# Kernel tuning notes

Measured on AMD Instinct MI355X. Metric: run time of the kernel, lower is better.

The kernel has to match this reference:

```python
import jax, jax.numpy as jnp
import numpy as np

B, NQ, C = 4, 3136, 512
H_IMG, W_IMG = 56, 56
HEADS, D_MODEL, D_K, D_V = 8, 512, 512, 512
RATIO = 2
LN_EPS = 1e-3   # keras LayerNormalization default
BN_EPS = 1e-3   # keras BatchNormalization default


def setup_inputs() -> dict:
    key = jax.random.key(0)
    ks = jax.random.split(key, 16)
    s = 0.02
    inp = {
        'queries': jax.random.normal(ks[0], (B, NQ, C), jnp.float32),
        'keys': jax.random.normal(ks[1], (B, NQ, C), jnp.float32),
        'values': jax.random.normal(ks[2], (B, NQ, C), jnp.float32),
        'Wq': jax.random.normal(ks[3], (C, HEADS * D_K), jnp.float32) * s,
        'bq': jnp.zeros((HEADS * D_K,), jnp.float32),
        'Wk': jax.random.normal(ks[4], (C, HEADS * D_K), jnp.float32) * s,
        'bk': jnp.zeros((HEADS * D_K,), jnp.float32),
        'Wv': jax.random.normal(ks[5], (C, HEADS * D_V), jnp.float32) * s,
        'bv': jnp.zeros((HEADS * D_V,), jnp.float32),
        'Wo': jax.random.normal(ks[6], (HEADS * D_V, D_MODEL), jnp.float32) * s,
        'bo': jnp.zeros((D_MODEL,), jnp.float32),
        # depthwise conv: kernel (kh, kw, in_per_group=1, out=C)
        'sr_kernel': jax.random.normal(ks[7], (RATIO + 1, RATIO + 1, 1, C), jnp.float32) * s,
        'sr_bias': jnp.zeros((C,), jnp.float32),
        'ln_gamma': jnp.ones((C,), jnp.float32),
        'ln_beta': jnp.zeros((C,), jnp.float32),
        # 1x1 channels_first conv over the head axis of the score tensor
        'tw': jax.random.normal(ks[8], (HEADS, HEADS), jnp.float32) * s,
        'tb': jnp.zeros((HEADS,), jnp.float32),
        # BatchNormalization(axis=[0,1]) -> params per (batch, head)
        'bn_gamma': jnp.ones((B, HEADS), jnp.float32),
        'bn_beta': jnp.zeros((B, HEADS), jnp.float32),
    }
    return inp


def _forward(queries, keys, values, Wq, bq, Wk, bk, Wv, bv, Wo, bo,
             sr_kernel, sr_bias, ln_gamma, ln_beta, tw, tb, bn_gamma, bn_beta):
    b, nq, c = queries.shape
    # Q projection -> (b, h, nq, d_model)  (d_k == d_model)
    q = (queries @ Wq + bq).reshape(b, nq, HEADS, D_MODEL).transpose(0, 2, 1, 3)
    # spatial reduction of K/V source (ratio > 1 path; keys/values args unused)
    x = queries.reshape(b, H_IMG, W_IMG, c)
    x = jax.lax.conv_general_dilated(
        x, sr_kernel, window_strides=(RATIO, RATIO), padding='SAME',
        dimension_numbers=('NHWC', 'HWIO', 'NHWC'), feature_group_count=c) + sr_bias
    x = x.reshape(b, -1, c)  # (b, nk, c), nk = (H/ratio)*(W/ratio)
    mu = jnp.mean(x, axis=-1, keepdims=True)
    var = jnp.mean(jnp.square(x - mu), axis=-1, keepdims=True)
    x = (x - mu) * jax.lax.rsqrt(var + LN_EPS) * ln_gamma + ln_beta
    k = (x @ Wk + bk).reshape(b, -1, HEADS, D_MODEL).transpose(0, 2, 1, 3)
    v = (x @ Wv + bv).reshape(b, -1, HEADS, D_MODEL).transpose(0, 2, 1, 3)
    # scores (b, h, nq, nk)
    att = jnp.einsum('bhqd,bhkd->bhqk', q, k) / np.sqrt(D_K).astype(np.float32)
    # transform: 1x1 conv over head channel, softmax over k, BN over (q, k)
    att = jnp.einsum('bhqk,hg->bgqk', att, tw) + tb[:, None, None]
    att = jax.nn.softmax(att, axis=-1)
    m = jnp.mean(att, axis=(2, 3), keepdims=True)
    s2 = jnp.mean(jnp.square(att - m), axis=(2, 3), keepdims=True)
    att = bn_gamma[:, :, None, None] * (att - m) * jax.lax.rsqrt(s2 + BN_EPS) \
          + bn_beta[:, :, None, None]
    # attend and project out
    out = jnp.einsum('bhqk,bhkd->bhqd', att, v)
    out = out.transpose(0, 2, 1, 3).reshape(b, nq, HEADS * D_V)
    return out @ Wo + bo


def reference(queries, keys, values, Wq, bq, Wk, bk, Wv, bv, Wo, bo,
              sr_kernel, sr_bias, ln_gamma, ln_beta, tw, tb, bn_gamma, bn_beta):
    return _forward(queries, keys, values, Wq, bq, Wk, bk, Wv, bv, Wo, bo,
                    sr_kernel, sr_bias, ln_gamma, ln_beta, tw, tb, bn_gamma, bn_beta)
```

## Files before the change

### kernel.cpp

```cpp
#include <hip/hip_runtime.h>
#include <hip/hip_bf16.h>
#include <math.h>

typedef unsigned short u16;
typedef __attribute__((ext_vector_type(4))) float f32x4;
typedef __attribute__((ext_vector_type(8))) __bf16 bf16x8;

#define B_    4
#define NQ_   3136
#define C_    512
#define HIMG  56
#define WIMG  56
#define HD_   4096
#define NK_   784
#define NKP_  832

static __device__ __forceinline__ float b2f(u16 u){
  union { unsigned int i; float f; } v; v.i = ((unsigned int)u)<<16; return v.f;
}
static __device__ __forceinline__ u16 f2b(float f){
  union { float f; unsigned int i; } v; v.f = f;
  unsigned int r = v.i + 0x7fffu + ((v.i>>16)&1u);
  return (u16)(r>>16);
}

#define GLD16(gsrc, ldst) __builtin_amdgcn_global_load_lds( \
    (const __attribute__((address_space(1))) void*)(gsrc), \
    (__attribute__((address_space(3))) void*)(ldst), 16, 0, 0)

static __device__ __forceinline__ void xcd_swz(int &bx, int &by, int &bz){
  const long nx = gridDim.x, ny = gridDim.y, nz = gridDim.z;
  const long l = blockIdx.x + nx*(blockIdx.y + ny*(long)blockIdx.z);
  const long n = nx*ny*nz;
  const long q8 = n>>3, r8 = n&7;
  const long xcd = l&7, idx = l>>3;
  const long wg = (xcd<r8 ? xcd*(q8+1) : r8*(q8+1) + (xcd-r8)*q8) + idx;
  by = (int)(wg % ny);
  bx = (int)((wg/ny) % nx);
  bz = (int)(wg/(nx*ny));
}

template<int OUT_F32>
__global__ __launch_bounds__(256)
void gemm128(const u16* __restrict__ A, const u16* __restrict__ Bm, void* __restrict__ Cm,
             int M, int Ncols, int K, int sA, int sB, int sC, int zdiv,
             long long zA1, long long zA2, long long zB1, long long zB2,
             long long zC1, long long zC2,
             const float* __restrict__ bias1, float hscale,
             const float* __restrict__ scalePtr,
             const float* __restrict__ bias2, int rowsPerB, int b2s)
{
  __shared__ u16 lds[32768];
  int bx, by, z;
  xcd_swz(bx, by, z);
  const int zq = z / zdiv, zr = z % zdiv;
  const u16* Ab = A  + (long long)zq*zA1 + (long long)zr*zA2;
  const u16* Bb = Bm + (long long)zq*zB1 + (long long)zr*zB2;
  const int m0 = bx*128, n0 = by*128;
  const int t = threadIdx.x, w = t>>6, lane = t&63;
  const int wm = w>>1, wn = w&1;
  const int l15 = lane & 15;

  const int srow = t>>3;
  const int scol = (((t&7) ^ (srow&7)) << 3);
  const u16* aS = Ab + (long long)(m0 + srow)*sA + scol;
  const u16* bS = Bb + (long long)(n0 + srow)*sB + scol;
  const long long sA32 = (long long)32*sA, sB32 = (long long)32*sB;
  const int w512 = w*512;

#define STAGE(jt, buf) do{                                        \
    const u16* a0_ = aS + (long long)(jt)*64;                     \
    const u16* b0_ = bS + (long long)(jt)*64;                     \
    u16* la_ = lds + (buf)*8192 + w512;                           \
    u16* lb_ = lds + 16384 + (buf)*8192 + w512;                   \
    GLD16(a0_,            la_);                                   \
    GLD16(a0_ +   sA32,   la_ + 2048);                            \
    GLD16(a0_ + 2*sA32,   la_ + 4096);                            \
    GLD16(a0_ + 3*sA32,   la_ + 6144);                            \
    GLD16(b0_,            lb_);                                   \
    GLD16(b0_ +   sB32,   lb_ + 2048);                            \
    GLD16(b0_ + 2*sB32,   lb_ + 4096);                            \
    GLD16(b0_ + 3*sB32,   lb_ + 6144);                            \
  }while(0)

  f32x4 acc[4][4];
#pragma unroll
  for(int i=0;i<4;i++)
#pragma unroll
    for(int j=0;j<4;j++) acc[i][j] = (f32x4)(0.0f);

  const char* ldsc = (const char*)lds;
  const int ck0 = (((lane>>4)     ^ (lane&7)) << 4);
  const int ck1 = (((4+(lane>>4)) ^ (lane&7)) << 4);
  const int aRowB = (wm*64 + l15) * 128;
  const int bRowB = (wn*64 + l15) * 128;

  const int T = K >> 6;
  STAGE(0, 0);
  STAGE(1, 1);

  for(int j=0; j<T; j++){
    const int bj = j & 1;
    if(j == T-1) asm volatile("s_waitcnt vmcnt(0)" ::: "memory");
    else         asm volatile("s_waitcnt vmcnt(8)" ::: "memory");
    asm volatile("s_barrier" ::: "memory");

    const int aBuf = bj*16384 + aRowB;
    const int bBuf = 32768 + bj*16384 + bRowB;
    {
      bf16x8 af[4], bf[4];
#pragma unroll
      for(int fr=0; fr<4; fr++) af[fr] = *(const bf16x8*)(ldsc + aBuf + fr*2048 + ck0);
#pragma unroll
      for(int fn=0; fn<4; fn++) bf[fn] = *(const bf16x8*)(ldsc + bBuf + fn*2048 + ck0);
      __builtin_amdgcn_s_setprio(1);
#pragma unroll
      for(int fr=0; fr<4; fr++)
#pragma unroll
        for(int fn=0; fn<4; fn++)
          acc[fr][fn] = __builtin_amdgcn_mfma_f32_16x16x32_bf16(af[fr], bf[fn], acc[fr][fn], 0,0,0);
      __builtin_amdgcn_s_setprio(0);
    }
    {
      bf16x8 af[4], bf[4];
#pragma unroll
      for(int fr=0; fr<4; fr++) af[fr] = *(const bf16x8*)(ldsc + aBuf + fr*2048 + ck1);
#pragma unroll
      for(int fn=0; fn<4; fn++) bf[fn] = *(const bf16x8*)(ldsc + bBuf + fn*2048 + ck1);
      __builtin_amdgcn_s_setprio(1);
#pragma unroll
      for(int fr=0; fr<4; fr++)
#pragma unroll
        for(int fn=0; fn<4; fn++)
          acc[fr][fn] = __builtin_amdgcn_mfma_f32_16x16x32_bf16(af[fr], bf[fn], acc[fr][fn], 0,0,0);
      __builtin_amdgcn_s_setprio(0);
    }
    asm volatile("s_barrier" ::: "memory");
    if(j+2 < T) STAGE(j+2, bj);
  }
#undef STAGE

  const float dsc = scalePtr ? scalePtr[z] : 1.0f;
  const long long cBase = (long long)zq*zC1 + (long long)zr*zC2;
  const int r4 = (lane>>4)*4;
#pragma unroll
  for(int mf=0; mf<4; mf++){
    const int row0 = m0 + wm*64 + mf*16 + r4;
#pragma unroll
    for(int nf=0; nf<4; nf++){
      const int col = n0 + wn*64 + nf*16 + l15;
      if(col < Ncols){
#pragma unroll
        for(int r=0;r<4;r++){
          const int row = row0 + r;
          if(row < M){
            float v = acc[mf][nf][r];
            if(bias1) v += bias1[col];
            v *= hscale * dsc;
            if(bias2) v += bias2[(row/rowsPerB)*b2s + col];
            if(OUT_F32) ((float*)Cm)[cBase + (long long)row*sC + col] = v;
            else        ((u16*) Cm)[cBase + (long long)row*sC + col] = f2b(v);
          }
        }
      }
    }
  }
}

__global__ __launch_bounds__(256)
void wt_kernel(const float* __restrict__ W, u16* __restrict__ Wt, int K, int N){
  __shared__ float tile[32][33];
  const int n0 = blockIdx.x*32, k0 = blockIdx.y*32;
  const int t = threadIdx.x, tr = t>>5, tc = t&31;
#pragma unroll
  for(int i=0;i<4;i++)
    tile[tr+i*8][tc] = W[(long long)(k0+tr+i*8)*N + n0+tc];
  __syncthreads();
#pragma unroll
  for(int i=0;i<4;i++)
    Wt[(long long)(n0+tr+i*8)*K + k0+tc] = f2b(tile[tc][tr+i*8]);
}

__global__ __launch_bounds__(256)
void cvt_bf16(const float* __restrict__ in, u16* __restrict__ outp, long long n){
  long long i = ((long long)blockIdx.x*256 + threadIdx.x)*4;
  if(i+3 < n){
    float4 v = *(const float4*)(in+i);
    ushort4 o; o.x=f2b(v.x); o.y=f2b(v.y); o.z=f2b(v.z); o.w=f2b(v.w);
    *(ushort4*)(outp+i) = o;
  }
}

__global__ __launch_bounds__(256)
void conv_ln(const float* __restrict__ q, const float* __restrict__ ker,
             const float* __restrict__ cbias, const float* __restrict__ gamma,
             const float* __restrict__ beta, u16* __restrict__ xo)
{
  const int p = blockIdx.x;
  const int b = p / 784, pix = p % 784;
  const int oy = pix / 28, ox = pix % 28;
  const int t = threadIdx.x;
  __shared__ float red[256];
  float v[2];
#pragma unroll
  for(int e=0;e<2;e++){
    const int c = t + e*256;
    float acc = cbias[c];
    for(int ky=0;ky<3;ky++){
      const int y = oy*2 + ky;
      if(y >= HIMG) continue;
      for(int kx=0;kx<3;kx++){
        const int x = ox*2 + kx;
        if(x >= WIMG) continue;
        acc += q[(((long long)b*HIMG + y)*WIMG + x)*C_ + c] * ker[(ky*3+kx)*C_ + c];
      }
    }
    v[e] = acc;
  }
  red[t]=v[0]+v[1]; __syncthreads();
  for(int st=128; st>0; st>>=1){ if(t<st) red[t]+=red[t+st]; __syncthreads(); }
  const float mu = red[0] * (1.0f/C_);
  __syncthreads();
  const float d0=v[0]-mu, d1=v[1]-mu;
  red[t]=d0*d0+d1*d1; __syncthreads();
  for(int st=128; st>0; st>>=1){ if(t<st) red[t]+=red[t+st]; __syncthreads(); }
  const float rs = rsqrtf(red[0]*(1.0f/C_) + 1e-3f);
  const long long ob = (long long)p*C_;
#pragma unroll
  for(int e=0;e<2;e++){
    const int c = t+e*256;
    xo[ob+c] = f2b((v[e]-mu)*rs*gamma[c] + beta[c]);
  }
}

__global__ __launch_bounds__(256)
void vt_kernel(const u16* __restrict__ Vf_b, u16* __restrict__ Vt_b, int sV){
  __shared__ u16 tile[32][33];
  const int k0 = blockIdx.x*32, d0 = blockIdx.y*32;
  const int t = threadIdx.x, tr = t>>5, tc = t&31;
#pragma unroll
  for(int i=0;i<4;i++){
    const int k = k0+tr+i*8;
    tile[tr+i*8][tc] = (k < NK_) ? Vf_b[(long long)k*sV + d0+tc] : (u16)0;
  }
  __syncthreads();
#pragma unroll
  for(int i=0;i<4;i++)
    Vt_b[(long long)(d0+tr+i*8)*NKP_ + k0+tc] = tile[tc][tr+i*8];
}

__global__ __launch_bounds__(512)
void mix_softmax(u16* __restrict__ S_b, const float* __restrict__ tw,
                 float* __restrict__ partial_b)
{
  const int qi = blockIdx.x;
  const int t = threadIdx.x;
  const int wave = t >> 6, lane = t & 63;
  __shared__ float sv[8*NK_];
  const long long rowstr = (long long)NQ_*NKP_;
  const long long base = (long long)qi*NKP_;

  for(int idx = t; idx < 8*196; idx += 512){
    const int h = idx / 196, c4 = idx % 196;
    ushort4 u4 = *(const ushort4*)(S_b + base + h*rowstr + c4*4);
    float* d = sv + h*NK_ + c4*4;
    d[0]=b2f(u4.x); d[1]=b2f(u4.y); d[2]=b2f(u4.z); d[3]=b2f(u4.w);
  }
  __syncthreads();

  const int g = wave;
  float wgt[8];
#pragma unroll
  for(int h=0;h<8;h++) wgt[h] = tw[h*8+g];

  float xs[13];
  float lmax = -1e30f;
#pragma unroll
  for(int j=0;j<13;j++){
    const int k = j*64 + lane;
    if(k < NK_){
      float x = 0.f;
#pragma unroll
      for(int h=0;h<8;h++) x += wgt[h]*sv[h*NK_+k];
      xs[j] = x;
      lmax = fmaxf(lmax, x);
    } else xs[j] = -1e30f;
  }
#pragma unroll
  for(int off=32; off>=1; off>>=1) lmax = fmaxf(lmax, __shfl_xor(lmax, off));

  float lsum = 0.f;
#pragma unroll
  for(int j=0;j<13;j++){
    const int k = j*64 + lane;
    if(k < NK_){
      const float e = __expf(xs[j] - lmax);
      xs[j] = e; lsum += e;
    }
  }
#pragma unroll
  for(int off=32; off>=1; off>>=1) lsum += __shfl_xor(lsum, off);
  const float inv = 1.0f/lsum;

  u16* dst = S_b + base + g*rowstr;
  float lss = 0.f;
#pragma unroll
  for(int j=0;j<13;j++){
    const int k = j*64 + lane;
    if(k < NK_){
      const float dev = xs[j]*inv - (1.0f/NK_);
      dst[k] = f2b(dev);
      lss += dev*dev;
    }
  }
  for(int k = NK_ + lane; k < NKP_; k += 64) dst[k] = 0;
#pragma unroll
  for(int off=32; off>=1; off>>=1) lss += __shfl_xor(lss, off);
  if(lane==0) partial_b[g*NQ_ + qi] = lss;
}

__global__ __launch_bounds__(256)
void colsum_v(const u16* __restrict__ Vf_b, float* __restrict__ cs_b, int sV){
  const int hd = blockIdx.x*256 + threadIdx.x;
  const u16* p = Vf_b + hd;
  float s=0.f;
  for(int k=0;k<NK_;k++) s += b2f(p[(long long)k*sV]);
  cs_b[hd]=s;
}

__global__ __launch_bounds__(256)
void finalize_stats(const float* __restrict__ partial_b, const float* __restrict__ bng_b,
                    const float* __restrict__ bnb_b, float* __restrict__ a_b,
                    float* __restrict__ c_b){
  const int g = blockIdx.x;
  const int t = threadIdx.x;
  __shared__ float red[4];
  float s = 0.f;
  for(int i=t; i<NQ_; i+=256) s += partial_b[g*NQ_ + i];
#pragma unroll
  for(int off=32; off>=1; off>>=1) s += __shfl_xor(s, off);
  if((t&63)==0) red[t>>6] = s;
  __syncthreads();
  if(t==0){
    const float tot = red[0]+red[1]+red[2]+red[3];
    const float s2 = tot * (1.0f/((float)NQ_*(float)NK_));
    a_b[g] = bng_b[g]*rsqrtf(s2 + 1e-3f);
    c_b[g] = bnb_b[g];
  }
}

__global__ __launch_bounds__(256)
void corr_kernel(const float* __restrict__ cs_b, const u16* __restrict__ Wot,
                 const float* __restrict__ c_b, float* __restrict__ corr_b){
  const int n = blockIdx.x, t = threadIdx.x;
  __shared__ float red[256];
  float s = 0.f;
  for(int hd=t; hd<HD_; hd+=256)
    s += c_b[hd>>9] * cs_b[hd] * b2f(Wot[(long long)n*HD_+hd]);
  red[t]=s; __syncthreads();
  for(int st=128; st>0; st>>=1){ if(t<st) red[t]+=red[t+st]; __syncthreads(); }
  if(t==0) corr_b[n]=red[0];
}

extern "C" void kernel_launch(void* const* d_in, const int* in_sizes, int n_in,
                              void* d_out, int out_size, void* d_ws, size_t ws_size,
                              hipStream_t stream)
{
  (void)in_sizes; (void)n_in; (void)out_size;
  const float* queries = (const float*)d_in[0];
  const float* Wq  = (const float*)d_in[3];
  const float* bq  = (const float*)d_in[4];
  const float* Wk  = (const float*)d_in[5];
  const float* bk  = (const float*)d_in[6];
  const float* Wv  = (const float*)d_in[7];
  const float* bv  = (const float*)d_in[8];
  const float* Wo  = (const float*)d_in[9];
  const float* bo  = (const float*)d_in[10];
  const float* srk = (const float*)d_in[11];
  const float* srb = (const float*)d_in[12];
  const float* lng = (const float*)d_in[13];
  const float* lnb = (const float*)d_in[14];
  const float* tw  = (const float*)d_in[15];
  const float* bng = (const float*)d_in[17];
  const float* bnb = (const float*)d_in[18];
  float* out = (float*)d_out;
  const float QSC = 0.04419417382415922f;

  char* w = (char*)d_ws;
  size_t off = 0;
  auto alloc = [&](size_t bytes)->char*{
    char* p = w + off; off += (bytes + 255) & ~(size_t)255; return p;
  };

  const bool tierA = (ws_size >= (size_t)210*1024*1024);

  u16* Wqt = (u16*)alloc((size_t)HD_*C_*2);
  u16* Wkt = (u16*)alloc((size_t)HD_*C_*2);
  u16* Wvt = (u16*)alloc((size_t)HD_*C_*2);
  u16* Wot = (u16*)alloc((size_t)C_*HD_*2);
  u16* x   = (u16*)alloc((size_t)B_*NK_*C_*2 + 262144);
  float* bkv = (float*)alloc((size_t)2*HD_*4);
  u16* Qin;
  u16* QfU;
  if(tierA){
    Qin = (u16*)alloc((size_t)B_*NQ_*C_*2);
    QfU = (u16*)alloc((size_t)B_*NQ_*HD_*2);
  } else {
    Qin = (u16*)alloc((size_t)NQ_*C_*2 + 262144);
    QfU = (u16*)alloc((size_t)NQ_*HD_*2);
  }
  u16* KV_b = (u16*)alloc((size_t)NK_*2*HD_*2 + 4194304);
  u16* Vt_b = (u16*)alloc((size_t)HD_*NKP_*2);
  u16* S_b  = (u16*)alloc((size_t)8*NQ_*NKP_*2 + 524288);
  float* colsum  = (float*)alloc((size_t)B_*HD_*4);
  float* partial = (float*)alloc((size_t)8*NQ_*4);
  float* aArr    = (float*)alloc(256);
  float* cArr    = (float*)alloc(256);
  float* corrB   = (float*)alloc((size_t)B_*C_*4);

  wt_kernel<<<dim3(128,16), 256, 0, stream>>>(Wq, Wqt, 512, 4096);
  wt_kernel<<<dim3(128,16), 256, 0, stream>>>(Wk, Wkt, 512, 4096);
  wt_kernel<<<dim3(128,16), 256, 0, stream>>>(Wv, Wvt, 512, 4096);
  wt_kernel<<<dim3(16,128), 256, 0, stream>>>(Wo, Wot, 4096, 512);
  conv_ln<<<B_*NK_, 256, 0, stream>>>(queries, srk, srb, lng, lnb, x);
  hipMemcpyAsync(bkv,      bk, HD_*4, hipMemcpyDeviceToDevice, stream);
  hipMemcpyAsync(bkv+HD_,  bv, HD_*4, hipMemcpyDeviceToDevice, stream);

  if(tierA){
    cvt_bf16<<<6272, 256, 0, stream>>>(queries, Qin, (long long)B_*NQ_*C_);
    gemm128<0><<<dim3(98,32,1),256,0,stream>>>(Qin, Wqt, QfU, B_*NQ_, 4096, 512,
        512, 512, HD_, 1, 0,0,0,0,0,0, bq, QSC, nullptr, nullptr, 1, 0);
  }

  for(int b=0; b<B_; b++){
    u16* Qf_b = tierA ? (QfU + (size_t)b*NQ_*HD_) : QfU;
    if(!tierA){
      cvt_bf16<<<1568, 256, 0, stream>>>(queries + (size_t)b*NQ_*C_, Qin, (long long)NQ_*C_);
      gemm128<0><<<dim3(25,32,1),256,0,stream>>>(Qin, Wqt, Qf_b, NQ_, 4096, 512,
          512, 512, HD_, 1, 0,0,0,0,0,0, bq, QSC, nullptr, nullptr, 1, 0);
    }
    const u16* x_b = x + (size_t)b*NK_*C_;
    gemm128<0><<<dim3(7,64,1),256,0,stream>>>(x_b, Wkt, KV_b, NK_, 2*HD_, 512,
        512, 512, 2*HD_, 1, 0,0,0,0,0,0, bkv, 1.0f, nullptr, nullptr, 1, 0);
    vt_kernel<<<dim3(26,128),256,0,stream>>>(KV_b + HD_, Vt_b, 2*HD_);
    colsum_v<<<16,256,0,stream>>>(KV_b + HD_, colsum + b*HD_, 2*HD_);
    gemm128<0><<<dim3(25,7,8),256,0,stream>>>(Qf_b, KV_b, S_b, NQ_, NKP_, 512,
        HD_, 2*HD_, NKP_, 8, 0, 512, 0, 512, 0, (long long)NQ_*NKP_,
        nullptr, 1.0f, nullptr, nullptr, 1, 0);
    mix_softmax<<<NQ_, 512, 0, stream>>>(S_b, tw, partial);
    finalize_stats<<<8,256,0,stream>>>(partial, bng + b*8, bnb + b*8, aArr + b*8, cArr + b*8);
    corr_kernel<<<512,256,0,stream>>>(colsum + b*HD_, Wot, cArr + b*8, corrB + b*C_);
    gemm128<0><<<dim3(25,4,8),256,0,stream>>>(S_b, Vt_b, Qf_b, NQ_, 512, NKP_,
        NKP_, NKP_, HD_, 8, 0, (long long)NQ_*NKP_, 0, (long long)512*NKP_, 0, 512,
        nullptr, 1.0f, aArr + b*8, nullptr, 1, 0);
    if(!tierA){
      gemm128<1><<<dim3(25,4,1),256,0,stream>>>(Qf_b, Wot, out + (size_t)b*NQ_*C_,
          NQ_, 512, HD_, HD_, HD_, C_,
          1, 0,0,0,0,0,0, bo, 1.0f, nullptr, corrB + b*C_, NQ_, C_);
    }
  }

  if(tierA){
    gemm128<1><<<dim3(98,4,1),256,0,stream>>>(QfU, Wot, out, B_*NQ_, 512, HD_,
        HD_, HD_, C_, 1, 0,0,0,0,0,0, bo, 1.0f, nullptr, corrB, NQ_, C_);
  }
}
```

Baseline: 1.008 ms.

## Switch GEMM to BK=32 four-buffer pipeline, simplify XCD remap, split colsum

The bf16 GEMM now uses a K-step of 32 with four LDS buffers and three stages in flight. The next stage is issued right after the fragment loads, which removes the second barrier per iteration and should hide global-load latency better. The XCD block remap is simplified and only reorders blocks when the block count divides by 8. colsum_v is split over 8 K-chunks so it launches more blocks, and corr_kernel sums the partials. The costs are more loop iterations and barriers per unit of K, and a new LDS swizzle whose correctness has to hold.

```diff
diff --git a/kernel.cpp b/kernel.cpp
--- a/kernel.cpp
+++ b/kernel.cpp
@@ -28,16 +28,14 @@
     (const __attribute__((address_space(1))) void*)(gsrc), \
     (__attribute__((address_space(3))) void*)(ldst), 16, 0, 0)
 
-static __device__ __forceinline__ void xcd_swz(int &bx, int &by, int &bz){
-  const long nx = gridDim.x, ny = gridDim.y, nz = gridDim.z;
-  const long l = blockIdx.x + nx*(blockIdx.y + ny*(long)blockIdx.z);
-  const long n = nx*ny*nz;
-  const long q8 = n>>3, r8 = n&7;
-  const long xcd = l&7, idx = l>>3;
-  const long wg = (xcd<r8 ? xcd*(q8+1) : r8*(q8+1) + (xcd-r8)*q8) + idx;
-  by = (int)(wg % ny);
-  bx = (int)((wg/ny) % nx);
-  bz = (int)(wg/(nx*ny));
+static __device__ __forceinline__ void xcd_order(int &bx, int &by, int &bz){
+  const int nx = gridDim.x, ny = gridDim.y, nz = gridDim.z;
+  long l = blockIdx.x + (long)nx*(blockIdx.y + (long)ny*blockIdx.z);
+  const long n = (long)nx*ny*nz;
+  long g = ((n&7)==0) ? ((l&7)*(n>>3) + (l>>3)) : l;
+  by = (int)(g % ny); g /= ny;
+  bx = (int)(g % nx);
+  bz = (int)(g / nx);
 }
 
 template<int OUT_F32>
@@ -52,7 +50,7 @@
 {
   __shared__ u16 lds[32768];
   int bx, by, z;
-  xcd_swz(bx, by, z);
+  xcd_order(bx, by, z);
   const int zq = z / zdiv, zr = z % zdiv;
   const u16* Ab = A  + (long long)zq*zA1 + (long long)zr*zA2;
   const u16* Bb = Bm + (long long)zq*zB1 + (long long)zr*zB2;
@@ -61,26 +59,22 @@
   const int wm = w>>1, wn = w&1;
   const int l15 = lane & 15;
 
-  const int srow = t>>3;
-  const int scol = (((t&7) ^ (srow&7)) << 3);
+  const int srow = t>>2;
+  const int scol = (((t&3) ^ ((srow>>1)&3)) << 3);
   const u16* aS = Ab + (long long)(m0 + srow)*sA + scol;
   const u16* bS = Bb + (long long)(n0 + srow)*sB + scol;
-  const long long sA32 = (long long)32*sA, sB32 = (long long)32*sB;
+  const long long sA64 = (long long)64*sA, sB64 = (long long)64*sB;
   const int w512 = w*512;
 
 #define STAGE(jt, buf) do{                                        \
-    const u16* a0_ = aS + (long long)(jt)*64;                     \
-    const u16* b0_ = bS + (long long)(jt)*64;                     \
-    u16* la_ = lds + (buf)*8192 + w512;                           \
-    u16* lb_ = lds + 16384 + (buf)*8192 + w512;                   \
-    GLD16(a0_,            la_);                                   \
-    GLD16(a0_ +   sA32,   la_ + 2048);                            \
-    GLD16(a0_ + 2*sA32,   la_ + 4096);                            \
-    GLD16(a0_ + 3*sA32,   la_ + 6144);                            \
-    GLD16(b0_,            lb_);                                   \
-    GLD16(b0_ +   sB32,   lb_ + 2048);                            \
-    GLD16(b0_ + 2*sB32,   lb_ + 4096);                            \
-    GLD16(b0_ + 3*sB32,   lb_ + 6144);                            \
+    const u16* a0_ = aS + (long long)(jt)*32;                     \
+    const u16* b0_ = bS + (long long)(jt)*32;                     \
+    u16* la_ = lds + (buf)*4096 + w512;                           \
+    u16* lb_ = lds + 16384 + (buf)*4096 + w512;                   \
+    GLD16(a0_,          la_);                                     \
+    GLD16(a0_ + sA64,   la_ + 2048);                              \
+    GLD16(b0_,          lb_);                                     \
+    GLD16(b0_ + sB64,   lb_ + 2048);                              \
   }while(0)
 
   f32x4 acc[4][4];
@@ -90,53 +84,37 @@
     for(int j=0;j<4;j++) acc[i][j] = (f32x4)(0.0f);
 
   const char* ldsc = (const char*)lds;
-  const int ck0 = (((lane>>4)     ^ (lane&7)) << 4);
-  const int ck1 = (((4+(lane>>4)) ^ (lane&7)) << 4);
-  const int aRowB = (wm*64 + l15) * 128;
-  const int bRowB = (wn*64 + l15) * 128;
-
-  const int T = K >> 6;
+  const int ck = (((lane>>4) ^ ((lane>>1)&3)) << 4);
+  const int aRowB = (wm*64 + l15) * 64;
+  const int bRowB = (wn*64 + l15) * 64;
+
+  const int T = K >> 5;
   STAGE(0, 0);
   STAGE(1, 1);
+  STAGE(2, 2);
 
   for(int j=0; j<T; j++){
-    const int bj = j & 1;
-    if(j == T-1) asm volatile("s_waitcnt vmcnt(0)" ::: "memory");
-    else         asm volatile("s_waitcnt vmcnt(8)" ::: "memory");
+    const int buf = j & 3;
+    if(j+2 < T)      asm volatile("s_waitcnt vmcnt(8)" ::: "memory");
+    else if(j+1 < T) asm volatile("s_waitcnt vmcnt(4)" ::: "memory");
+    else             asm volatile("s_waitcnt vmcnt(0)" ::: "memory");
     asm volatile("s_barrier" ::: "memory");
 
-    const int aBuf = bj*16384 + aRowB;
-    const int bBuf = 32768 + bj*16384 + bRowB;
-    {
-      bf16x8 af[4], bf[4];
-#pragma unroll
-      for(int fr=0; fr<4; fr++) af[fr] = *(const bf16x8*)(ldsc + aBuf + fr*2048 + ck0);
-#pragma unroll
-      for(int fn=0; fn<4; fn++) bf[fn] = *(const bf16x8*)(ldsc + bBuf + fn*2048 + ck0);
-      __builtin_amdgcn_s_setprio(1);
-#pragma unroll
-      for(int fr=0; fr<4; fr++)
-#pragma unroll
-        for(int fn=0; fn<4; fn++)
-          acc[fr][fn] = __builtin_amdgcn_mfma_f32_16x16x32_bf16(af[fr], bf[fn], acc[fr][fn], 0,0,0);
-      __builtin_amdgcn_s_setprio(0);
-    }
-    {
-      bf16x8 af[4], bf[4];
-#pragma unroll
-      for(int fr=0; fr<4; fr++) af[fr] = *(const bf16x8*)(ldsc + aBuf + fr*2048 + ck1);
-#pragma unroll
-      for(int fn=0; fn<4; fn++) bf[fn] = *(const bf16x8*)(ldsc + bBuf + fn*2048 + ck1);
-      __builtin_amdgcn_s_setprio(1);
-#pragma unroll
-      for(int fr=0; fr<4; fr++)
-#pragma unroll
-        for(int fn=0; fn<4; fn++)
-          acc[fr][fn] = __builtin_amdgcn_mfma_f32_16x16x32_bf16(af[fr], bf[fn], acc[fr][fn], 0,0,0);
-      __builtin_amdgcn_s_setprio(0);
-    }
-    asm volatile("s_barrier" ::: "memory");
-    if(j+2 < T) STAGE(j+2, bj);
+    const int aBuf = buf*8192 + aRowB;
+    const int bBuf = 32768 + buf*8192 + bRowB;
+    bf16x8 af[4], bfv[4];
+#pragma unroll
+    for(int fr=0; fr<4; fr++) af[fr]  = *(const bf16x8*)(ldsc + aBuf + fr*1024 + ck);
+#pragma unroll
+    for(int fn=0; fn<4; fn++) bfv[fn] = *(const bf16x8*)(ldsc + bBuf + fn*1024 + ck);
+    if(j+3 < T) STAGE(j+3, (j+3)&3);
+    __builtin_amdgcn_s_setprio(1);
+#pragma unroll
+    for(int fr=0; fr<4; fr++)
+#pragma unroll
+      for(int fn=0; fn<4; fn++)
+        acc[fr][fn] = __builtin_amdgcn_mfma_f32_16x16x32_bf16(af[fr], bfv[fn], acc[fr][fn], 0,0,0);
+    __builtin_amdgcn_s_setprio(0);
   }
 #undef STAGE
 
@@ -320,12 +298,13 @@
 }
 
 __global__ __launch_bounds__(256)
-void colsum_v(const u16* __restrict__ Vf_b, float* __restrict__ cs_b, int sV){
+void colsum_v(const u16* __restrict__ Vf_b, float* __restrict__ part, int sV){
   const int hd = blockIdx.x*256 + threadIdx.x;
-  const u16* p = Vf_b + hd;
+  const int kc = blockIdx.y;
+  const u16* p = Vf_b + (long long)kc*98*sV + hd;
   float s=0.f;
-  for(int k=0;k<NK_;k++) s += b2f(p[(long long)k*sV]);
-  cs_b[hd]=s;
+  for(int k=0;k<98;k++) s += b2f(p[(long long)k*sV]);
+  part[(long long)kc*HD_ + hd] = s;
 }
 
 __global__ __launch_bounds__(256)
@@ -350,13 +329,17 @@
 }
 
 __global__ __launch_bounds__(256)
-void corr_kernel(const float* __restrict__ cs_b, const u16* __restrict__ Wot,
+void corr_kernel(const float* __restrict__ part, const u16* __restrict__ Wot,
                  const float* __restrict__ c_b, float* __restrict__ corr_b){
   const int n = blockIdx.x, t = threadIdx.x;
   __shared__ float red[256];
   float s = 0.f;
-  for(int hd=t; hd<HD_; hd+=256)
-    s += c_b[hd>>9] * cs_b[hd] * b2f(Wot[(long long)n*HD_+hd]);
+  for(int hd=t; hd<HD_; hd+=256){
+    float cs = 0.f;
+#pragma unroll
+    for(int kc=0; kc<8; kc++) cs += part[(long long)kc*HD_ + hd];
+    s += c_b[hd>>9] * cs * b2f(Wot[(long long)n*HD_+hd]);
+  }
   red[t]=s; __syncthreads();
   for(int st=128; st>0; st>>=1){ if(t<st) red[t]+=red[t+st]; __syncthreads(); }
   if(t==0) corr_b[n]=red[0];
@@ -412,7 +395,7 @@
   u16* KV_b = (u16*)alloc((size_t)NK_*2*HD_*2 + 4194304);
   u16* Vt_b = (u16*)alloc((size_t)HD_*NKP_*2);
   u16* S_b  = (u16*)alloc((size_t)8*NQ_*NKP_*2 + 524288);
-  float* colsum  = (float*)alloc((size_t)B_*HD_*4);
+  float* colsum  = (float*)alloc((size_t)8*HD_*4);
   float* partial = (float*)alloc((size_t)8*NQ_*4);
   float* aArr    = (float*)alloc(256);
   float* cArr    = (float*)alloc(256);
@@ -443,13 +426,13 @@
     gemm128<0><<<dim3(7,64,1),256,0,stream>>>(x_b, Wkt, KV_b, NK_, 2*HD_, 512,
         512, 512, 2*HD_, 1, 0,0,0,0,0,0, bkv, 1.0f, nullptr, nullptr, 1, 0);
     vt_kernel<<<dim3(26,128),256,0,stream>>>(KV_b + HD_, Vt_b, 2*HD_);
-    colsum_v<<<16,256,0,stream>>>(KV_b + HD_, colsum + b*HD_, 2*HD_);
+    colsum_v<<<dim3(16,8),256,0,stream>>>(KV_b + HD_, colsum, 2*HD_);
     gemm128<0><<<dim3(25,7,8),256,0,stream>>>(Qf_b, KV_b, S_b, NQ_, NKP_, 512,
         HD_, 2*HD_, NKP_, 8, 0, 512, 0, 512, 0, (long long)NQ_*NKP_,
         nullptr, 1.0f, nullptr, nullptr, 1, 0);
     mix_softmax<<<NQ_, 512, 0, stream>>>(S_b, tw, partial);
     finalize_stats<<<8,256,0,stream>>>(partial, bng + b*8, bnb + b*8, aArr + b*8, cArr + b*8);
-    corr_kernel<<<512,256,0,stream>>>(colsum + b*HD_, Wot, cArr + b*8, corrB + b*C_);
+    corr_kernel<<<512,256,0,stream>>>(colsum, Wot, cArr + b*8, corrB + b*C_);
     gemm128<0><<<dim3(25,4,8),256,0,stream>>>(S_b, Vt_b, Qf_b, NQ_, 512, NKP_,
         NKP_, NKP_, HD_, 8, 0, (long long)NQ_*NKP_, 0, (long long)512*NKP_, 0, 512,
         nullptr, 1.0f, aArr + b*8, nullptr, 1, 0);
```

Result: faster. 910.8 us (-9.6%).
